# Performance work log

Hardware: AMD Instinct MI355X
Metric: run time of the kernel (lower is better)

## Reference

```python
import jax, jax.numpy as jnp
import numpy as np

N_ENTITY = 100000
H_DIM = 512
N_ROWS = 262144
ALPHA = 0.5          # EMA rate for fast state
GATE_TH = 0.5        # gate_threshold buffer
GATE_SCALE = 5.0     # gate_scale buffer
LN_EPS = 1e-5


def setup_inputs() -> dict:
    key = jax.random.key(0)
    k1, k2, k3, k4, k5 = jax.random.split(key, 5)
    entity_emb = jax.random.normal(k1, (N_ROWS, H_DIM), dtype=jnp.float32)
    entity_ids = jax.random.randint(k2, (N_ROWS,), 0, N_ENTITY, dtype=jnp.int64)
    slow_state = 0.1 * jax.random.normal(k3, (N_ENTITY, H_DIM), dtype=jnp.float32)
    fast_state = 0.1 * jax.random.normal(k4, (N_ENTITY, H_DIM), dtype=jnp.float32)
    # torch nn.Linear(2h, h): weight shape (h, 2h), y = x @ W.T + b
    W = jax.random.normal(k5, (H_DIM, 2 * H_DIM), dtype=jnp.float32) * 0.02
    b = jnp.zeros((H_DIM,), dtype=jnp.float32)
    return {"entity_emb": entity_emb, "slow_state": slow_state,
            "fast_state": fast_state, "W": W, "b": b, "entity_ids": entity_ids}


def _layer_norm(x):
    mu = jnp.mean(x, axis=-1, keepdims=True)
    var = jnp.mean(jnp.square(x - mu), axis=-1, keepdims=True)
    return (x - mu) * jax.lax.rsqrt(var + LN_EPS)


def reference(entity_emb, slow_state, fast_state, W, b, entity_ids):
    # ---- fuse_with_state (gate path) ----
    state = slow_state[entity_ids]                                   # (N, h) gather
    is_active = (jnp.sum(jnp.abs(state), axis=-1, keepdims=True) > 1e-6).astype(entity_emb.dtype)
    h_state = _layer_norm(state)
    gate_in = jnp.concatenate([entity_emb, h_state], axis=-1)        # (N, 2h)
    z = jax.nn.sigmoid(gate_in @ W.T + b)                            # (N, h)
    fused = z * entity_emb + (1.0 - z) * h_state
    out = is_active * fused + (1.0 - is_active) * entity_emb

    # ---- writeback (no-grad in torch; scatter-reduce EMA + norm-gated slow update) ----
    ctx = jax.lax.stop_gradient(out)
    ids = entity_ids
    counts = jax.ops.segment_sum(jnp.ones((ctx.shape[0],), ctx.dtype), ids,
                                 num_segments=N_ENTITY)              # (E,)
    ctx_sum = jax.ops.segment_sum(ctx, ids, num_segments=N_ENTITY)   # (E, h)
    ctx_mean = ctx_sum / jnp.clip(counts, 1.0)[:, None]
    touched = (counts > 0)[:, None]
    new_fast_all = (1.0 - ALPHA) * fast_state + ALPHA * ctx_mean
    new_fast = jnp.where(touched, new_fast_all, fast_state)
    diff = new_fast - slow_state
    delta = jnp.linalg.norm(diff, axis=-1, keepdims=True)
    gate = jax.nn.sigmoid(GATE_SCALE * (delta - GATE_TH))
    new_slow = jnp.where(touched, slow_state + gate * diff, slow_state)
    return out, new_fast, new_slow
```

## Files before the change

kernel.cpp:

```cpp
#include <hip/hip_runtime.h>
#include <hip/hip_bf16.h>
#include <cstdint>

#define NROWS 262144
#define HDIM  512
#define NENT  100000
#define SCAN_NBLK ((NENT + 1023) / 1024)

typedef __attribute__((ext_vector_type(4))) float  f32x4;
typedef __attribute__((ext_vector_type(8))) short  bf16x8;

static __device__ __forceinline__ unsigned short f2bf(float x) {
    unsigned u = __float_as_uint(x);
    u += 0x7FFF + ((u >> 16) & 1);
    return (unsigned short)(u >> 16);
}
static __device__ __forceinline__ float bf2f(unsigned short h) {
    unsigned u = ((unsigned)h) << 16;
    return __uint_as_float(u);
}

__global__ void pack_w_kernel(const float* __restrict__ W, unsigned short* __restrict__ Wp) {
    int g    = blockIdx.x * 256 + threadIdx.x;
    int lane = g & 63;
    int task = g >> 6;
    int nt   = task >> 5;
    int kt   = task & 31;
    int col  = nt * 16 + (lane & 15);
    int k    = kt * 32 + ((lane >> 4) << 3);
    const float* src = W + (size_t)col * 1024 + k;
    f32x4 v0 = *(const f32x4*)(src);
    f32x4 v1 = *(const f32x4*)(src + 4);
    bf16x8 ov;
#pragma unroll
    for (int i = 0; i < 4; ++i) {
        ov[i]     = (short)f2bf(v0[i]);
        ov[4 + i] = (short)f2bf(v1[i]);
    }
    *(bf16x8*)(Wp + (size_t)g * 8) = ov;
}

__global__ __launch_bounds__(256) void count_kernel(const int* __restrict__ ids,
                                                    unsigned* __restrict__ counts) {
    int r = blockIdx.x * 256 + threadIdx.x;
    if (r < NROWS) atomicAdd(&counts[ids[r]], 1u);
}

__global__ __launch_bounds__(1024) void scan1_kernel(const unsigned* __restrict__ counts,
                                                     unsigned* __restrict__ off,
                                                     unsigned* __restrict__ bsums) {
    __shared__ unsigned tmp[1024];
    int i = blockIdx.x * 1024 + threadIdx.x;
    unsigned v = (i < NENT) ? counts[i] : 0u;
    tmp[threadIdx.x] = v;
    __syncthreads();
#pragma unroll
    for (int o = 1; o < 1024; o <<= 1) {
        unsigned a = (threadIdx.x >= o) ? tmp[threadIdx.x - o] : 0u;
        __syncthreads();
        tmp[threadIdx.x] += a;
        __syncthreads();
    }
    if (i < NENT) off[i] = tmp[threadIdx.x] - v;
    if (threadIdx.x == 1023) bsums[blockIdx.x] = tmp[1023];
}

__global__ void scan2_kernel(unsigned* __restrict__ bsums) {
    if (threadIdx.x == 0 && blockIdx.x == 0) {
        unsigned s = 0;
        for (int i = 0; i < SCAN_NBLK; ++i) { unsigned t = bsums[i]; bsums[i] = s; s += t; }
    }
}

__global__ __launch_bounds__(1024) void scan3_kernel(unsigned* __restrict__ off,
                                                     const unsigned* __restrict__ bsums,
                                                     unsigned* __restrict__ cursor) {
    int i = blockIdx.x * 1024 + threadIdx.x;
    if (i < NENT) {
        unsigned o = off[i] + bsums[blockIdx.x];
        off[i] = o;
        cursor[i] = o;
    }
    if (i == 0) off[NENT] = NROWS;
}

__global__ __launch_bounds__(256) void fill_kernel(const int* __restrict__ ids,
                                                   unsigned* __restrict__ cursor,
                                                   int* __restrict__ rowidx) {
    int r = blockIdx.x * 256 + threadIdx.x;
    if (r < NROWS) {
        unsigned p = atomicAdd(&cursor[ids[r]], 1u);
        rowidx[p] = r;
    }
}

__global__ __launch_bounds__(512, 4) void fuse_kernel(
    const float* __restrict__ emb, const float* __restrict__ slow,
    const unsigned short* __restrict__ Wp, const float* __restrict__ bias,
    const int* __restrict__ ids, float* __restrict__ out)
{
    __shared__ unsigned short xLds[64 * 64 * 8];
    __shared__ float muS[32], rsS[32], actS[32], bS[512];
    __shared__ int idS[32];

    const int t    = threadIdx.x;
    const int w    = t >> 6;
    const int lane = t & 63;
    const int brow = blockIdx.x * 32;

    if (t < 128) ((f32x4*)bS)[t] = ((const f32x4*)bias)[t];

    for (int rr = 0; rr < 4; ++rr) {
        int row = w * 4 + rr;
        int id  = ids[brow + row];
        const float* sp = slow + (size_t)id * HDIM;
        f32x4 v0 = ((const f32x4*)sp)[lane * 2];
        f32x4 v1 = ((const f32x4*)sp)[lane * 2 + 1];
        float s = 0.f, s2 = 0.f, sa = 0.f;
#pragma unroll
        for (int i = 0; i < 4; ++i) {
            s  += v0[i] + v1[i];
            s2 += v0[i] * v0[i] + v1[i] * v1[i];
            sa += fabsf(v0[i]) + fabsf(v1[i]);
        }
#pragma unroll
        for (int m = 32; m >= 1; m >>= 1) {
            s  += __shfl_xor(s, m);
            s2 += __shfl_xor(s2, m);
            sa += __shfl_xor(sa, m);
        }
        if (lane == 0) {
            float mu  = s * (1.f / HDIM);
            float var = s2 * (1.f / HDIM) - mu * mu;
            muS[row]  = mu;
            rsS[row]  = rsqrtf(var + 1e-5f);
            actS[row] = (sa > 1e-6f) ? 1.f : 0.f;
            idS[row]  = id;
        }
    }
    __syncthreads();

    for (int slot = t; slot < 4096; slot += 512) {
        int T    = slot >> 6;
        int ls   = slot & 63;
        int kt   = T >> 1;
        int row  = (T & 1) * 16 + (ls & 15);
        int k    = kt * 32 + ((ls >> 4) << 3);
        f32x4 x0, x1;
        if (k < 512) {
            const float* p = emb + (size_t)(brow + row) * HDIM + k;
            x0 = *(const f32x4*)p;
            x1 = *(const f32x4*)(p + 4);
        } else {
            const float* p = slow + (size_t)idS[row] * HDIM + (k - 512);
            x0 = *(const f32x4*)p;
            x1 = *(const f32x4*)(p + 4);
            float mu = muS[row], rs = rsS[row];
#pragma unroll
            for (int i = 0; i < 4; ++i) {
                x0[i] = (x0[i] - mu) * rs;
                x1[i] = (x1[i] - mu) * rs;
            }
        }
        bf16x8 av;
#pragma unroll
        for (int i = 0; i < 4; ++i) {
            av[i]     = (short)f2bf(x0[i]);
            av[4 + i] = (short)f2bf(x1[i]);
        }
        ((bf16x8*)xLds)[slot] = av;
    }
    __syncthreads();

    f32x4 zero4 = {0.f, 0.f, 0.f, 0.f};
    f32x4 acc[2][4];
#pragma unroll
    for (int i = 0; i < 2; ++i)
#pragma unroll
        for (int j = 0; j < 4; ++j) acc[i][j] = zero4;

    const unsigned short* wpL = Wp + (size_t)lane * 8;

#define LOADW(dst, kt)                                                  \
    _Pragma("unroll")                                                   \
    for (int ct = 0; ct < 4; ++ct)                                      \
        dst[ct] = *(const bf16x8*)(wpL + ((size_t)((w * 4 + ct) * 32 + (kt)) << 9));

#define LOADX(dst, kt)                                                  \
    _Pragma("unroll")                                                   \
    for (int rt = 0; rt < 2; ++rt)                                      \
        dst[rt] = ((const bf16x8*)xLds)[((kt) * 2 + rt) * 64 + lane];

#define MFMA_STEP(wf, xf)                                               \
    _Pragma("unroll")                                                   \
    for (int ct = 0; ct < 4; ++ct) {                                    \
        acc[0][ct] = __builtin_amdgcn_mfma_f32_16x16x32_bf16(wf[ct], xf[0], acc[0][ct], 0, 0, 0); \
        acc[1][ct] = __builtin_amdgcn_mfma_f32_16x16x32_bf16(wf[ct], xf[1], acc[1][ct], 0, 0, 0); \
    }

    bf16x8 wA[4], wB[4], xA[2], xB[2];
    LOADW(wA, 0);
    LOADX(xA, 0);
    for (int kt = 0; kt < 32; kt += 2) {
        if (kt + 1 < 32) { LOADW(wB, kt + 1); LOADX(xB, kt + 1); }
        MFMA_STEP(wA, xA);
        if (kt + 2 < 32) { LOADW(wA, kt + 2); LOADX(xA, kt + 2); }
        if (kt + 1 < 32) MFMA_STEP(wB, xB);
    }
#undef LOADW
#undef LOADX
#undef MFMA_STEP

#pragma unroll
    for (int rt = 0; rt < 2; ++rt) {
        int rowl = rt * 16 + (lane & 15);
        int grow = brow + rowl;
        float mu = muS[rowl], rs = rsS[rowl], act = actS[rowl];
        (void)mu; (void)rs;
        float* outP = out + (size_t)grow * HDIM;
#pragma unroll
        for (int ct = 0; ct < 4; ++ct) {
            int col0 = w * 64 + ct * 16 + ((lane >> 4) << 2);
            int Te = ((col0 >> 5) * 2 + rt) * 64 + (((col0 >> 3) & 3) << 4) + (lane & 15);
            const unsigned short* pe = xLds + Te * 8 + (col0 & 7);
            int kh = 512 + col0;
            int Th = ((kh >> 5) * 2 + rt) * 64 + (((kh >> 3) & 3) << 4) + (lane & 15);
            const unsigned short* ph = xLds + Th * 8 + (kh & 7);
            f32x4 bv = *(const f32x4*)&bS[col0];
            f32x4 o;
#pragma unroll
            for (int r = 0; r < 4; ++r) {
                float ev = bf2f(pe[r]);
                float hv = bf2f(ph[r]);
                float logit = acc[rt][ct][r] + bv[r];
                float z  = 1.f / (1.f + __expf(-logit));
                float fused = z * ev + (1.f - z) * hv;
                o[r] = (act > 0.f) ? fused : ev;
            }
            *(f32x4*)(outP + col0) = o;
        }
    }
}

__global__ __launch_bounds__(256) void finalize_kernel(
    const float* __restrict__ fast, const float* __restrict__ slow,
    const float* __restrict__ out, const unsigned* __restrict__ off,
    const int* __restrict__ rowidx, float* __restrict__ nf, float* __restrict__ ns)
{
    int e = blockIdx.x * 4 + (threadIdx.x >> 6);
    if (e >= NENT) return;
    int lane = threadIdx.x & 63;
    size_t base = (size_t)e * HDIM + lane * 8;

    f32x4 f0 = *(const f32x4*)(fast + base), f1 = *(const f32x4*)(fast + base + 4);
    f32x4 l0 = *(const f32x4*)(slow + base), l1 = *(const f32x4*)(slow + base + 4);

    unsigned o0 = off[e], o1 = off[e + 1];
    int c = (int)(o1 - o0);

    if (c == 0) {
        *(f32x4*)(nf + base)     = f0;
        *(f32x4*)(nf + base + 4) = f1;
        *(f32x4*)(ns + base)     = l0;
        *(f32x4*)(ns + base + 4) = l1;
        return;
    }

    f32x4 s0 = {0.f, 0.f, 0.f, 0.f}, s1 = {0.f, 0.f, 0.f, 0.f};
    for (int j = 0; j < c; ++j) {
        int r = rowidx[o0 + j];
        const float* p = out + (size_t)r * HDIM + lane * 8;
        s0 += *(const f32x4*)p;
        s1 += *(const f32x4*)(p + 4);
    }

    float inv = 0.5f / (float)c;
    f32x4 n0, n1, d0, d1;
    float ss = 0.f;
#pragma unroll
    for (int i = 0; i < 4; ++i) {
        n0[i] = 0.5f * f0[i] + s0[i] * inv;
        n1[i] = 0.5f * f1[i] + s1[i] * inv;
        d0[i] = n0[i] - l0[i]; ss += d0[i] * d0[i];
        d1[i] = n1[i] - l1[i]; ss += d1[i] * d1[i];
    }
#pragma unroll
    for (int m = 32; m >= 1; m >>= 1) ss += __shfl_xor(ss, m);
    float delta = sqrtf(ss);
    float gate  = 1.f / (1.f + expf(-5.f * (delta - 0.5f)));

    f32x4 o0v, o1v;
#pragma unroll
    for (int i = 0; i < 4; ++i) {
        o0v[i] = l0[i] + gate * d0[i];
        o1v[i] = l1[i] + gate * d1[i];
    }
    *(f32x4*)(nf + base)     = n0;
    *(f32x4*)(nf + base + 4) = n1;
    *(f32x4*)(ns + base)     = o0v;
    *(f32x4*)(ns + base + 4) = o1v;
}

extern "C" void kernel_launch(void* const* d_in, const int* in_sizes, int n_in,
                              void* d_out, int out_size, void* d_ws, size_t ws_size,
                              hipStream_t stream) {
    const float* emb  = (const float*)d_in[0];
    const float* slow = (const float*)d_in[1];
    const float* fast = (const float*)d_in[2];
    const float* W    = (const float*)d_in[3];
    const float* bias = (const float*)d_in[4];
    const int*   ids  = (const int*)d_in[5];

    float* out = (float*)d_out;
    float* nf  = out + (size_t)NROWS * HDIM;
    float* ns  = nf + (size_t)NENT * HDIM;

    unsigned short* Wp   = (unsigned short*)d_ws;
    unsigned* counts     = (unsigned*)((char*)d_ws + (1u << 20));
    unsigned* off        = (unsigned*)((char*)d_ws + (1u << 20) + 512 * 1024);
    unsigned* bsums      = (unsigned*)((char*)d_ws + (2u << 20));
    int*      rowidx     = (int*)((char*)d_ws + (2u << 20) + 4096);

    hipMemsetAsync(counts, 0, (size_t)NENT * sizeof(unsigned), stream);

    pack_w_kernel<<<256, 256, 0, stream>>>(W, Wp);
    count_kernel<<<NROWS / 256, 256, 0, stream>>>(ids, counts);
    scan1_kernel<<<SCAN_NBLK, 1024, 0, stream>>>(counts, off, bsums);
    scan2_kernel<<<1, 64, 0, stream>>>(bsums);
    scan3_kernel<<<SCAN_NBLK, 1024, 0, stream>>>(off, bsums, counts);
    fill_kernel<<<NROWS / 256, 256, 0, stream>>>(ids, counts, rowidx);
    fuse_kernel<<<NROWS / 32, 512, 0, stream>>>(emb, slow, Wp, bias, ids, out);
    finalize_kernel<<<(NENT + 3) / 4, 256, 0, stream>>>(fast, slow, out, off, rowidx, nf, ns);
}
```

Measured before the change: 941.8 us.

## Reorder packed W per wave and deepen MFMA load pipeline to four stages

Repacks the bf16 weight buffer so each wave's four column tiles for a given k-step sit contiguously, which makes weight loads per wave sequential. The GEMM loop moves from double buffering to a fully unrolled four-deep register prefetch so global weight loads have more time to complete before their MFMAs issue. Launch bounds drop from 4 to 3 blocks per SM to give the extra prefetch buffers register room, at the cost of lower occupancy. An unused mu/rs load is also removed.

```diff
diff --git a/kernel.cpp b/kernel.cpp
--- a/kernel.cpp
+++ b/kernel.cpp
@@ -23,9 +23,10 @@
 __global__ void pack_w_kernel(const float* __restrict__ W, unsigned short* __restrict__ Wp) {
     int g    = blockIdx.x * 256 + threadIdx.x;
     int lane = g & 63;
-    int task = g >> 6;
-    int nt   = task >> 5;
-    int kt   = task & 31;
+    int ct   = (g >> 6) & 3;
+    int kt   = (g >> 8) & 31;
+    int w    = g >> 13;
+    int nt   = w * 4 + ct;
     int col  = nt * 16 + (lane & 15);
     int k    = kt * 32 + ((lane >> 4) << 3);
     const float* src = W + (size_t)col * 1024 + k;
@@ -94,7 +95,7 @@
     }
 }
 
-__global__ __launch_bounds__(512, 4) void fuse_kernel(
+__global__ __launch_bounds__(512, 3) void fuse_kernel(
     const float* __restrict__ emb, const float* __restrict__ slow,
     const unsigned short* __restrict__ Wp, const float* __restrict__ bias,
     const int* __restrict__ ids, float* __restrict__ out)
@@ -179,44 +180,53 @@
 #pragma unroll
         for (int j = 0; j < 4; ++j) acc[i][j] = zero4;
 
-    const unsigned short* wpL = Wp + (size_t)lane * 8;
+    const unsigned short* wpW = Wp + (size_t)w * 65536 + (size_t)lane * 8;
+    const bf16x8* xBase = (const bf16x8*)xLds + lane;
 
 #define LOADW(dst, kt)                                                  \
-    _Pragma("unroll")                                                   \
-    for (int ct = 0; ct < 4; ++ct)                                      \
-        dst[ct] = *(const bf16x8*)(wpL + ((size_t)((w * 4 + ct) * 32 + (kt)) << 9));
-
+    {   _Pragma("unroll")                                               \
+        for (int ct = 0; ct < 4; ++ct)                                  \
+            dst[ct] = *(const bf16x8*)(wpW + ((kt) * 4 + ct) * 512);    \
+    }
 #define LOADX(dst, kt)                                                  \
-    _Pragma("unroll")                                                   \
-    for (int rt = 0; rt < 2; ++rt)                                      \
-        dst[rt] = ((const bf16x8*)xLds)[((kt) * 2 + rt) * 64 + lane];
-
-#define MFMA_STEP(wf, xf)                                               \
-    _Pragma("unroll")                                                   \
-    for (int ct = 0; ct < 4; ++ct) {                                    \
-        acc[0][ct] = __builtin_amdgcn_mfma_f32_16x16x32_bf16(wf[ct], xf[0], acc[0][ct], 0, 0, 0); \
-        acc[1][ct] = __builtin_amdgcn_mfma_f32_16x16x32_bf16(wf[ct], xf[1], acc[1][ct], 0, 0, 0); \
-    }
-
-    bf16x8 wA[4], wB[4], xA[2], xB[2];
-    LOADW(wA, 0);
-    LOADX(xA, 0);
-    for (int kt = 0; kt < 32; kt += 2) {
-        if (kt + 1 < 32) { LOADW(wB, kt + 1); LOADX(xB, kt + 1); }
-        MFMA_STEP(wA, xA);
-        if (kt + 2 < 32) { LOADW(wA, kt + 2); LOADX(xA, kt + 2); }
-        if (kt + 1 < 32) MFMA_STEP(wB, xB);
+    {   _Pragma("unroll")                                               \
+        for (int rt = 0; rt < 2; ++rt)                                  \
+            dst[rt] = xBase[((kt) * 2 + rt) * 64];                      \
+    }
+#define STEP(wf, xf)                                                    \
+    {   _Pragma("unroll")                                               \
+        for (int ct = 0; ct < 4; ++ct) {                                \
+            acc[0][ct] = __builtin_amdgcn_mfma_f32_16x16x32_bf16(wf[ct], xf[0], acc[0][ct], 0, 0, 0); \
+            acc[1][ct] = __builtin_amdgcn_mfma_f32_16x16x32_bf16(wf[ct], xf[1], acc[1][ct], 0, 0, 0); \
+        }                                                               \
+    }
+
+    bf16x8 wQ0[4], wQ1[4], wQ2[4], wQ3[4];
+    bf16x8 xQ0[2], xQ1[2], xQ2[2], xQ3[2];
+
+    LOADW(wQ0, 0); LOADX(xQ0, 0);
+    LOADW(wQ1, 1); LOADX(xQ1, 1);
+    LOADW(wQ2, 2); LOADX(xQ2, 2);
+#pragma unroll
+    for (int kt = 0; kt < 32; kt += 4) {
+        if (kt + 3 < 32) { LOADW(wQ3, kt + 3); LOADX(xQ3, kt + 3); }
+        STEP(wQ0, xQ0);
+        if (kt + 4 < 32) { LOADW(wQ0, kt + 4); LOADX(xQ0, kt + 4); }
+        STEP(wQ1, xQ1);
+        if (kt + 5 < 32) { LOADW(wQ1, kt + 5); LOADX(xQ1, kt + 5); }
+        STEP(wQ2, xQ2);
+        if (kt + 6 < 32) { LOADW(wQ2, kt + 6); LOADX(xQ2, kt + 6); }
+        STEP(wQ3, xQ3);
     }
 #undef LOADW
 #undef LOADX
-#undef MFMA_STEP
+#undef STEP
 
 #pragma unroll
     for (int rt = 0; rt < 2; ++rt) {
         int rowl = rt * 16 + (lane & 15);
         int grow = brow + rowl;
-        float mu = muS[rowl], rs = rsS[rowl], act = actS[rowl];
-        (void)mu; (void)rs;
+        float act = actS[rowl];
         float* outP = out + (size_t)grow * HDIM;
 #pragma unroll
         for (int ct = 0; ct < 4; ++ct) {
```

New measurement: 1.463 ms. +55.3%, slower.
